# Kernel optimization log

Hardware: AMD Instinct MI355X
Metric: run time of the kernel (lower is better)

Reference implementation:

```python
import jax, jax.numpy as jnp
import numpy as np

BETA = 10.0
EPS = 1e-6


def setup_inputs() -> dict:
    key = jax.random.key(0)
    k0, k1 = jax.random.split(key)
    f0 = jax.random.normal(k0, (4, 256, 64, 64), dtype=jnp.float32)
    f1 = jax.random.normal(k1, (4, 256, 64, 64), dtype=jnp.float32)
    return {"f0": f0, "f1": f1}


def _l2norm(x, axis):
    norm = jnp.sqrt(jnp.sum(x * x, axis=axis, keepdims=True))
    return x / jnp.maximum(norm, EPS)


def reference(f0, f1):
    B, C, Ha, Wa = f0.shape
    _, _, Hb, Wb = f1.shape
    # [B, HaWa, C] and [B, HbWb, C]
    a = f0.reshape(B, C, Ha * Wa).transpose(0, 2, 1)
    b = f1.reshape(B, C, Hb * Wb).transpose(0, 2, 1)
    a = _l2norm(a, axis=2)
    b = _l2norm(b, axis=2)
    # cosine similarity scaled by beta: [B, HaWa, HbWb]
    sim = jnp.einsum('bnc,bmc->bnm', a, b) * BETA
    attn = jax.nn.softmax(sim, axis=2)
    # target coords (x, y) of image1 grid: [HbWb, 2]
    ys = jnp.arange(Hb, dtype=f0.dtype)
    xs = jnp.arange(Wb, dtype=f0.dtype)
    yy, xx = jnp.meshgrid(ys, xs, indexing='ij')
    coords = jnp.stack([xx.reshape(-1), yy.reshape(-1)], axis=1)
    tgt = jnp.einsum('bnm,mk->bnk', attn, coords)
    warp_c = tgt.reshape(B, Ha, Wa, 2)
    cert_c = jnp.max(attn, axis=2).reshape(B, Ha, Wa)
    return (warp_c, cert_c)
```

## Files before the change

### kernel.cpp

```cpp
#include <hip/hip_runtime.h>
#include <hip/hip_bf16.h>

#define BETA_LOG2E 14.426950408889634f
#define EPSN 1e-6f

typedef __bf16 bf16x8 __attribute__((ext_vector_type(8)));
typedef float  f32x4  __attribute__((ext_vector_type(4)));

static __device__ inline unsigned short f2bf(float f) {
    __hip_bfloat16 h = __float2bfloat16(f);
    return __builtin_bit_cast(unsigned short, h);
}
static __device__ inline float bf2f(unsigned short u) {
    unsigned int b = ((unsigned int)u) << 16;
    return __builtin_bit_cast(float, b);
}

__global__ __launch_bounds__(256) void k_norm_transpose(
    const float* __restrict__ f0, const float* __restrict__ f1,
    unsigned short* __restrict__ aT, unsigned short* __restrict__ bT)
{
    __shared__ unsigned short tile[256][65];
    __shared__ float partial[4][64];
    __shared__ float inv_l[64];

    int idx   = blockIdx.x;
    int which = idx >> 8;
    int rem   = idx & 255;
    int b     = rem >> 6;
    int n0    = (rem & 63) * 64;
    const float* src = which ? f1 : f0;
    unsigned short* dst = which ? bT : aT;

    int t   = threadIdx.x;
    int n_l = t & 63;
    int cg  = t >> 6;

    float ss = 0.f;
#pragma unroll 4
    for (int i = 0; i < 64; ++i) {
        int c = i * 4 + cg;
        float v = src[(b * 256 + c) * 4096 + n0 + n_l];
        ss += v * v;
        tile[c][n_l] = f2bf(v);
    }
    partial[cg][n_l] = ss;
    __syncthreads();
    if (t < 64) {
        float s = partial[0][t] + partial[1][t] + partial[2][t] + partial[3][t];
        inv_l[t] = 1.0f / fmaxf(sqrtf(s), EPSN);
    }
    __syncthreads();

#pragma unroll 4
    for (int j = 0; j < 16; ++j) {
        int nw = (t & 3) + (j & 3) * 4 + (t >> 6) * 16;
        int u  = ((t >> 2) & 15) + (j >> 2) * 16;
        int c  = u * 4;
        float inv = inv_l[nw];
        unsigned short o0 = f2bf(bf2f(tile[c + 0][nw]) * inv);
        unsigned short o1 = f2bf(bf2f(tile[c + 1][nw]) * inv);
        unsigned short o2 = f2bf(bf2f(tile[c + 2][nw]) * inv);
        unsigned short o3 = f2bf(bf2f(tile[c + 3][nw]) * inv);
        uint2 val;
        val.x = (unsigned int)o0 | ((unsigned int)o1 << 16);
        val.y = (unsigned int)o2 | ((unsigned int)o3 << 16);
        *reinterpret_cast<uint2*>(&dst[((size_t)(b * 4096 + n0 + nw)) * 256 + c]) = val;
    }
}

__global__ __launch_bounds__(256) void k_flash(
    const unsigned short* __restrict__ aT, const unsigned short* __restrict__ bT,
    float* __restrict__ stats)
{
    __shared__ unsigned short kbuf[64 * 272];

    int idx   = blockIdx.x;
    int xcd   = idx & 7;
    int batch = xcd >> 1;
    int sub   = ((idx >> 3) << 1) | (xcd & 1);
    int qt    = sub >> 2;
    int ks    = sub & 3;

    int t    = threadIdx.x;
    int w    = t >> 6;
    int lane = t & 63;
    int quad = lane >> 4;
    int l15  = lane & 15;
    int q0w  = qt * 128 + w * 32;
    int k0   = ks * 1024;

    bf16x8 afrag[2][8];
#pragma unroll
    for (int s = 0; s < 2; ++s) {
        const unsigned short* ap =
            aT + ((size_t)(batch * 4096 + q0w + s * 16 + l15)) * 256 + quad * 8;
#pragma unroll
        for (int kk = 0; kk < 8; ++kk)
            afrag[s][kk] = *reinterpret_cast<const bf16x8*>(ap + kk * 32);
    }

    float Z[8], Sx[8], Sy[8], Pm[8];
#pragma unroll
    for (int i = 0; i < 8; ++i) { Z[i] = 0.f; Sx[i] = 0.f; Sy[i] = 0.f; Pm[i] = 0.f; }

    for (int ch = 0; ch < 16; ++ch) {
        int kbase = k0 + ch * 64;
        const unsigned short* gsrc = bT + ((size_t)(batch * 4096 + kbase)) * 256;
#pragma unroll
        for (int i = 0; i < 8; ++i) {
            int h = i * 2048 + t * 8;
            uint4 v = *reinterpret_cast<const uint4*>(gsrc + h);
            int key  = i * 8 + (t >> 5);
            int gran = t & 31;
            *reinterpret_cast<uint4*>(&kbuf[key * 272 + gran * 8]) = v;
        }
        __syncthreads();

#pragma unroll
        for (int nt = 0; nt < 4; ++nt) {
            f32x4 acc0 = {0.f, 0.f, 0.f, 0.f};
            f32x4 acc1 = {0.f, 0.f, 0.f, 0.f};
            const unsigned short* lp = &kbuf[(nt * 16 + l15) * 272 + quad * 8];
#pragma unroll
            for (int kk = 0; kk < 8; ++kk) {
                bf16x8 bfrag = *reinterpret_cast<const bf16x8*>(lp + kk * 32);
                acc0 = __builtin_amdgcn_mfma_f32_16x16x32_bf16(afrag[0][kk], bfrag, acc0, 0, 0, 0);
                acc1 = __builtin_amdgcn_mfma_f32_16x16x32_bf16(afrag[1][kk], bfrag, acc1, 0, 0, 0);
            }
            int key  = kbase + nt * 16 + l15;
            float kx = (float)(key & 63);
            float ky = (float)(key >> 6);
#pragma unroll
            for (int r = 0; r < 4; ++r) {
                float p0 = exp2f(acc0[r] * BETA_LOG2E);
                Z[r]  += p0;  Sx[r] += p0 * kx;  Sy[r] += p0 * ky;
                Pm[r] = fmaxf(Pm[r], p0);
                float p1 = exp2f(acc1[r] * BETA_LOG2E);
                Z[4 + r]  += p1;  Sx[4 + r] += p1 * kx;  Sy[4 + r] += p1 * ky;
                Pm[4 + r] = fmaxf(Pm[4 + r], p1);
            }
        }
        __syncthreads();
    }

#pragma unroll
    for (int i = 0; i < 8; ++i) {
#pragma unroll
        for (int m = 1; m <= 8; m <<= 1) {
            Z[i]  += __shfl_xor(Z[i], m);
            Sx[i] += __shfl_xor(Sx[i], m);
            Sy[i] += __shfl_xor(Sy[i], m);
            Pm[i]  = fmaxf(Pm[i], __shfl_xor(Pm[i], m));
        }
    }
    if (l15 == 0) {
#pragma unroll
        for (int s = 0; s < 2; ++s)
#pragma unroll
            for (int r = 0; r < 4; ++r) {
                int q = q0w + s * 16 + quad * 4 + r;
                f32x4 st = {Z[s * 4 + r], Sx[s * 4 + r], Sy[s * 4 + r], Pm[s * 4 + r]};
                *reinterpret_cast<f32x4*>(&stats[((size_t)(batch * 4096 + q) * 4 + ks) * 4]) = st;
            }
    }
}

__global__ __launch_bounds__(256) void k_finalize(
    const float* __restrict__ stats, float* __restrict__ out)
{
    int q = blockIdx.x * 256 + threadIdx.x;
    const f32x4* s = reinterpret_cast<const f32x4*>(stats + (size_t)q * 16);
    f32x4 a0 = s[0], a1 = s[1], a2 = s[2], a3 = s[3];
    float Z  = a0.x + a1.x + a2.x + a3.x;
    float Sx = a0.y + a1.y + a2.y + a3.y;
    float Sy = a0.z + a1.z + a2.z + a3.z;
    float Pm = fmaxf(fmaxf(a0.w, a1.w), fmaxf(a2.w, a3.w));
    float invZ = 1.0f / Z;
    out[q * 2 + 0]  = Sx * invZ;
    out[q * 2 + 1]  = Sy * invZ;
    out[32768 + q]  = Pm * invZ;
}

extern "C" void kernel_launch(void* const* d_in, const int* in_sizes, int n_in,
                              void* d_out, int out_size, void* d_ws, size_t ws_size,
                              hipStream_t stream)
{
    const float* f0 = (const float*)d_in[0];
    const float* f1 = (const float*)d_in[1];
    unsigned short* aT = (unsigned short*)d_ws;
    unsigned short* bT = aT + (size_t)4 * 4096 * 256;
    float* stats = (float*)(bT + (size_t)4 * 4096 * 256);
    float* out = (float*)d_out;

    hipLaunchKernelGGL(k_norm_transpose, dim3(512), dim3(256), 0, stream, f0, f1, aT, bT);
    hipLaunchKernelGGL(k_flash,          dim3(512), dim3(256), 0, stream, aT, bT, stats);
    hipLaunchKernelGGL(k_finalize,       dim3(64),  dim3(256), 0, stream, stats, out);
}
```

Baseline: 129.9 us.

## Vectorize norm-transpose, fold beta into queries, hoist ky per chunk, widen key split

Result: slower. 194.1 us (+49.4%).

```diff
diff --git a/kernel.cpp b/kernel.cpp
--- a/kernel.cpp
+++ b/kernel.cpp
@@ -7,71 +7,75 @@
 typedef __bf16 bf16x8 __attribute__((ext_vector_type(8)));
 typedef float  f32x4  __attribute__((ext_vector_type(4)));
 
-static __device__ inline unsigned short f2bf(float f) {
-    __hip_bfloat16 h = __float2bfloat16(f);
-    return __builtin_bit_cast(unsigned short, h);
-}
-static __device__ inline float bf2f(unsigned short u) {
-    unsigned int b = ((unsigned int)u) << 16;
-    return __builtin_bit_cast(float, b);
+static __device__ inline unsigned int pack2bf(float a, float b) {
+    __hip_bfloat16 ha = __float2bfloat16(a);
+    __hip_bfloat16 hb = __float2bfloat16(b);
+    return (unsigned int)__builtin_bit_cast(unsigned short, ha) |
+           ((unsigned int)__builtin_bit_cast(unsigned short, hb) << 16);
 }
 
 __global__ __launch_bounds__(256) void k_norm_transpose(
     const float* __restrict__ f0, const float* __restrict__ f1,
     unsigned short* __restrict__ aT, unsigned short* __restrict__ bT)
 {
-    __shared__ unsigned short tile[256][65];
-    __shared__ float partial[4][64];
-    __shared__ float inv_l[64];
+    __shared__ float tile[64 * 260];
+    __shared__ float partial[16 * 64];
+    __shared__ float scale_s[64];
 
     int idx   = blockIdx.x;
     int which = idx >> 8;
     int rem   = idx & 255;
     int b     = rem >> 6;
     int n0    = (rem & 63) * 64;
-    const float* src = which ? f1 : f0;
+    const float4* src4 = (const float4*)(which ? f1 : f0);
     unsigned short* dst = which ? bT : aT;
 
-    int t   = threadIdx.x;
-    int n_l = t & 63;
-    int cg  = t >> 6;
-
-    float ss = 0.f;
-#pragma unroll 4
-    for (int i = 0; i < 64; ++i) {
-        int c = i * 4 + cg;
-        float v = src[(b * 256 + c) * 4096 + n0 + n_l];
-        ss += v * v;
-        tile[c][n_l] = f2bf(v);
-    }
-    partial[cg][n_l] = ss;
+    int t  = threadIdx.x;
+    int n4 = t & 15;
+    int cg = t >> 4;
+
+    f32x4 ssv = {0.f, 0.f, 0.f, 0.f};
+#pragma unroll
+    for (int i = 0; i < 16; ++i) {
+        int c = i * 16 + cg;
+        float4 v = src4[(size_t)(b * 256 + c) * 1024 + (n0 >> 2) + n4];
+        tile[(n4 * 4 + 0) * 260 + c] = v.x;
+        tile[(n4 * 4 + 1) * 260 + c] = v.y;
+        tile[(n4 * 4 + 2) * 260 + c] = v.z;
+        tile[(n4 * 4 + 3) * 260 + c] = v.w;
+        ssv.x += v.x * v.x;  ssv.y += v.y * v.y;
+        ssv.z += v.z * v.z;  ssv.w += v.w * v.w;
+    }
+    *reinterpret_cast<f32x4*>(&partial[cg * 64 + n4 * 4]) = ssv;
     __syncthreads();
     if (t < 64) {
-        float s = partial[0][t] + partial[1][t] + partial[2][t] + partial[3][t];
-        inv_l[t] = 1.0f / fmaxf(sqrtf(s), EPSN);
+        float s = 0.f;
+#pragma unroll
+        for (int g = 0; g < 16; ++g) s += partial[g * 64 + t];
+        scale_s[t] = (which ? 1.0f : BETA_LOG2E) / fmaxf(sqrtf(s), EPSN);
     }
     __syncthreads();
 
-#pragma unroll 4
-    for (int j = 0; j < 16; ++j) {
-        int nw = (t & 3) + (j & 3) * 4 + (t >> 6) * 16;
-        int u  = ((t >> 2) & 15) + (j >> 2) * 16;
-        int c  = u * 4;
-        float inv = inv_l[nw];
-        unsigned short o0 = f2bf(bf2f(tile[c + 0][nw]) * inv);
-        unsigned short o1 = f2bf(bf2f(tile[c + 1][nw]) * inv);
-        unsigned short o2 = f2bf(bf2f(tile[c + 2][nw]) * inv);
-        unsigned short o3 = f2bf(bf2f(tile[c + 3][nw]) * inv);
-        uint2 val;
-        val.x = (unsigned int)o0 | ((unsigned int)o1 << 16);
-        val.y = (unsigned int)o2 | ((unsigned int)o3 << 16);
-        *reinterpret_cast<uint2*>(&dst[((size_t)(b * 4096 + n0 + nw)) * 256 + c]) = val;
-    }
-}
-
-__global__ __launch_bounds__(256) void k_flash(
+#pragma unroll
+    for (int it = 0; it < 8; ++it) {
+        int n    = it * 8 + (t >> 5);
+        int cgrp = t & 31;
+        float sc = scale_s[n];
+        const float* row = &tile[n * 260 + cgrp * 8];
+        float4 u = *reinterpret_cast<const float4*>(row);
+        float4 w = *reinterpret_cast<const float4*>(row + 4);
+        uint4 o;
+        o.x = pack2bf(u.x * sc, u.y * sc);
+        o.y = pack2bf(u.z * sc, u.w * sc);
+        o.z = pack2bf(w.x * sc, w.y * sc);
+        o.w = pack2bf(w.z * sc, w.w * sc);
+        *reinterpret_cast<uint4*>(&dst[(size_t)(b * 4096 + n0 + n) * 256 + cgrp * 8]) = o;
+    }
+}
+
+__global__ __launch_bounds__(256, 4) void k_flash(
     const unsigned short* __restrict__ aT, const unsigned short* __restrict__ bT,
-    float* __restrict__ stats)
+    float* __restrict__ stats, int nks, int lg)
 {
     __shared__ unsigned short kbuf[64 * 272];
 
@@ -79,8 +83,10 @@
     int xcd   = idx & 7;
     int batch = xcd >> 1;
     int sub   = ((idx >> 3) << 1) | (xcd & 1);
-    int qt    = sub >> 2;
-    int ks    = sub & 3;
+    int qt    = sub >> lg;
+    int ks    = sub & (nks - 1);
+    int kps   = 4096 >> lg;
+    int chunks = kps >> 6;
 
     int t    = threadIdx.x;
     int w    = t >> 6;
@@ -88,7 +94,7 @@
     int quad = lane >> 4;
     int l15  = lane & 15;
     int q0w  = qt * 128 + w * 32;
-    int k0   = ks * 1024;
+    int k0   = ks * kps;
 
     bf16x8 afrag[2][8];
 #pragma unroll
@@ -100,11 +106,13 @@
             afrag[s][kk] = *reinterpret_cast<const bf16x8*>(ap + kk * 32);
     }
 
-    float Z[8], Sx[8], Sy[8], Pm[8];
-#pragma unroll
-    for (int i = 0; i < 8; ++i) { Z[i] = 0.f; Sx[i] = 0.f; Sy[i] = 0.f; Pm[i] = 0.f; }
-
-    for (int ch = 0; ch < 16; ++ch) {
+    float Z[8], Sx[8], Sy[8], Pm[8], Zc[8];
+#pragma unroll
+    for (int i = 0; i < 8; ++i) { Z[i] = 0.f; Sx[i] = 0.f; Sy[i] = 0.f; Pm[i] = 0.f; Zc[i] = 0.f; }
+
+    float kxl = (float)l15;
+
+    for (int ch = 0; ch < chunks; ++ch) {
         int kbase = k0 + ch * 64;
         const unsigned short* gsrc = bT + ((size_t)(batch * 4096 + kbase)) * 256;
 #pragma unroll
@@ -128,20 +136,23 @@
                 acc0 = __builtin_amdgcn_mfma_f32_16x16x32_bf16(afrag[0][kk], bfrag, acc0, 0, 0, 0);
                 acc1 = __builtin_amdgcn_mfma_f32_16x16x32_bf16(afrag[1][kk], bfrag, acc1, 0, 0, 0);
             }
-            int key  = kbase + nt * 16 + l15;
-            float kx = (float)(key & 63);
-            float ky = (float)(key >> 6);
+            float kx = (float)(nt * 16) + kxl;
 #pragma unroll
             for (int r = 0; r < 4; ++r) {
-                float p0 = exp2f(acc0[r] * BETA_LOG2E);
-                Z[r]  += p0;  Sx[r] += p0 * kx;  Sy[r] += p0 * ky;
-                Pm[r] = fmaxf(Pm[r], p0);
-                float p1 = exp2f(acc1[r] * BETA_LOG2E);
-                Z[4 + r]  += p1;  Sx[4 + r] += p1 * kx;  Sy[4 + r] += p1 * ky;
-                Pm[4 + r] = fmaxf(Pm[4 + r], p1);
+                float p0 = exp2f(acc0[r]);
+                Z[r] += p0;  Sx[r] += p0 * kx;  Pm[r] = fmaxf(Pm[r], p0);
+                float p1 = exp2f(acc1[r]);
+                Z[4 + r] += p1;  Sx[4 + r] += p1 * kx;  Pm[4 + r] = fmaxf(Pm[4 + r], p1);
             }
         }
         __syncthreads();
+
+        float ky = (float)(ks * chunks + ch);
+#pragma unroll
+        for (int i = 0; i < 8; ++i) {
+            Sy[i] += ky * (Z[i] - Zc[i]);
+            Zc[i] = Z[i];
+        }
     }
 
 #pragma unroll
@@ -161,21 +172,22 @@
             for (int r = 0; r < 4; ++r) {
                 int q = q0w + s * 16 + quad * 4 + r;
                 f32x4 st = {Z[s * 4 + r], Sx[s * 4 + r], Sy[s * 4 + r], Pm[s * 4 + r]};
-                *reinterpret_cast<f32x4*>(&stats[((size_t)(batch * 4096 + q) * 4 + ks) * 4]) = st;
+                *reinterpret_cast<f32x4*>(
+                    &stats[((size_t)(batch * 4096 + q) * nks + ks) * 4]) = st;
             }
     }
 }
 
 __global__ __launch_bounds__(256) void k_finalize(
-    const float* __restrict__ stats, float* __restrict__ out)
+    const float* __restrict__ stats, float* __restrict__ out, int nks)
 {
     int q = blockIdx.x * 256 + threadIdx.x;
-    const f32x4* s = reinterpret_cast<const f32x4*>(stats + (size_t)q * 16);
-    f32x4 a0 = s[0], a1 = s[1], a2 = s[2], a3 = s[3];
-    float Z  = a0.x + a1.x + a2.x + a3.x;
-    float Sx = a0.y + a1.y + a2.y + a3.y;
-    float Sy = a0.z + a1.z + a2.z + a3.z;
-    float Pm = fmaxf(fmaxf(a0.w, a1.w), fmaxf(a2.w, a3.w));
+    const f32x4* s = reinterpret_cast<const f32x4*>(stats + (size_t)q * 4 * nks);
+    float Z = 0.f, Sx = 0.f, Sy = 0.f, Pm = 0.f;
+    for (int i = 0; i < nks; ++i) {
+        f32x4 a = s[i];
+        Z += a.x;  Sx += a.y;  Sy += a.z;  Pm = fmaxf(Pm, a.w);
+    }
     float invZ = 1.0f / Z;
     out[q * 2 + 0]  = Sx * invZ;
     out[q * 2 + 1]  = Sy * invZ;
@@ -193,7 +205,11 @@
     float* stats = (float*)(bT + (size_t)4 * 4096 * 256);
     float* out = (float*)d_out;
 
+    size_t base = (size_t)2 * 4 * 4096 * 256 * 2;
+    int nks = (ws_size >= base + (size_t)16384 * 8 * 16) ? 8 : 4;
+    int lg  = (nks == 8) ? 3 : 2;
+
     hipLaunchKernelGGL(k_norm_transpose, dim3(512), dim3(256), 0, stream, f0, f1, aT, bT);
-    hipLaunchKernelGGL(k_flash,          dim3(512), dim3(256), 0, stream, aT, bT, stats);
-    hipLaunchKernelGGL(k_finalize,       dim3(64),  dim3(256), 0, stream, stats, out);
-}
+    hipLaunchKernelGGL(k_flash, dim3(128 * nks), dim3(256), 0, stream, aT, bT, stats, nks, lg);
+    hipLaunchKernelGGL(k_finalize, dim3(64), dim3(256), 0, stream, stats, out, nks);
+}
```
